# Kernel optimization log

Measured on AMD Instinct MI355X. Metric: run time of the kernel, lower is better.

Reference implementation:

```python
import jax, jax.numpy as jnp
import numpy as np

K = 3  # hardcoded in DRKNN.__init__


def setup_inputs() -> dict:
    key = jax.random.key(0)
    k1, k2, k3 = jax.random.split(key, 3)
    N, Q, A, B = 100000, 1024, 8, 16
    dataTensorX = jax.random.normal(k1, (N, A, B), dtype=jnp.float32)
    dataTensorY = jax.random.normal(k2, (N, 3), dtype=jnp.float32)
    inputTensor = jax.random.normal(k3, (Q, A, B), dtype=jnp.float32)
    return {"dataTensorX": dataTensorX, "dataTensorY": dataTensorY, "inputTensor": inputTensor}


def reference(dataTensorX, dataTensorY, inputTensor):
    # Flatten feature dims (1,2) -> single feature axis F = A*B
    N = dataTensorX.shape[0]
    Q = inputTensor.shape[0]
    X = dataTensorX.reshape(N, -1)   # [N, F]
    Qf = inputTensor.reshape(Q, -1)  # [Q, F]
    # squared L2 distance via expansion: ||q||^2 - 2 q.x + ||x||^2 -> [Q, N]
    x2 = jnp.sum(X * X, axis=-1)     # [N]
    q2 = jnp.sum(Qf * Qf, axis=-1)   # [Q]
    dists = q2[:, None] - 2.0 * (Qf @ X.T) + x2[None, :]  # [Q, N]
    # k smallest distances == k largest of negated distances
    _, idx = jax.lax.top_k(-dists, K)  # idx: [Q, K] int32
    outs = dataTensorY[idx]            # [Q, K, label_dim]
    out = jnp.mean(outs, axis=1)       # [Q, label_dim]
    return out, idx
```

## Files before the change

kernel.cpp:

```cpp
#include <hip/hip_runtime.h>

#define F       128
#define TILE    128
#define QBLK    128
#define FQI     8
#define NCHUNKS 64
#define KSTEP   32
#define TOPK    3
#define NSUB_MAX 3200
#define DINF    (__builtin_inff())
#define IMAX    0x7fffffff

typedef short short8 __attribute__((ext_vector_type(8)));
typedef float f32x4  __attribute__((ext_vector_type(4)));

__device__ __forceinline__ ushort f2bf(float f) {
    uint u = __float_as_uint(f);
    uint r = (u + 0x7fffu + ((u >> 16) & 1u)) >> 16;
    return (ushort)r;
}

__device__ __forceinline__ bool lex_less(float d1, int i1, float d2, int i2) {
    return (d1 < d2) || (d1 == d2 && i1 < i2);
}

__device__ __forceinline__ void gload16(const ushort* g, ushort* l) {
    __builtin_amdgcn_global_load_lds(
        (const __attribute__((address_space(1))) uint*)g,
        (__attribute__((address_space(3))) uint*)l, 16, 0, 0);
}


__global__ void conv_kernel(const float* __restrict__ src, ushort* __restrict__ dst,
                            float* __restrict__ nrm, int rows, int rowsPad) {
    int row  = blockIdx.x * 4 + (threadIdx.x >> 6);
    int lane = threadIdx.x & 63;
    if (row >= rowsPad) return;
    if (row < rows) {
        float2 v = *reinterpret_cast<const float2*>(&src[(size_t)row * F + lane * 2]);
        ushort2 b; b.x = f2bf(v.x); b.y = f2bf(v.y);
        *reinterpret_cast<ushort2*>(&dst[(size_t)row * F + lane * 2]) = b;
        float s = v.x * v.x + v.y * v.y;
        #pragma unroll
        for (int m = 32; m >= 1; m >>= 1) s += __shfl_xor(s, m, 64);
        if (lane == 0) nrm[row] = s;
    } else {
        *reinterpret_cast<ushort2*>(&dst[(size_t)row * F + lane * 2]) = make_ushort2(0, 0);
        if (lane == 0) nrm[row] = DINF;
    }
}

__global__ __launch_bounds__(256) void knn_p1(
    const ushort* __restrict__ Xbf, const ushort* __restrict__ Qbf,
    const float* __restrict__ x2f, float* __restrict__ part,
    int NTILES, int NSUB)
{
    __shared__ ushort sX[2][16384];

    const int t   = threadIdx.x;
    const int W   = t >> 6;
    const int l   = t & 63;
    const int l15 = l & 15;
    const int g   = l >> 4;
    const int chunk = blockIdx.x;
    const int qbase = blockIdx.y * QBLK;
    const int tile0 = (int)(((long)chunk * NTILES) >> 6);
    const int tile1 = (int)(((long)(chunk + 1) * NTILES) >> 6);
    const int ntile = tile1 - tile0;

    auto stage = [&](int tile, int b) {
        const ushort* gbase = Xbf + (size_t)(tile * TILE + W * 32) * F;
        #pragma unroll
        for (int m = 0; m < 8; m++) {
            const ushort* gp = gbase + ((m & 1) * 16 + l15) * F + (m >> 1) * 32 + g * 8;
            gload16(gp, &sX[b][W * 4096 + m * 512]);
        }
    };

    stage(tile0, 0);

    short8 qf[FQI][4];
    #pragma unroll
    for (int fqi = 0; fqi < FQI; fqi++) {
        const ushort* qr = Qbf + (size_t)(qbase + fqi * 16 + l15) * F + g * 8;
        #pragma unroll
        for (int s = 0; s < 4; s++) {
            uint4 u = *reinterpret_cast<const uint4*>(qr + s * 32);
            qf[fqi][s] = *reinterpret_cast<short8*>(&u);
        }
    }

    asm volatile("s_waitcnt vmcnt(0)" ::: "memory");
    __builtin_amdgcn_sched_barrier(0);

    for (int i = 0; i < ntile; i++) {
        const int tile = tile0 + i;
        const int cb = i & 1;

        float4 xv0 = *reinterpret_cast<const float4*>(&x2f[(size_t)tile * TILE + W * 32 + g * 4]);
        float4 xv1 = *reinterpret_cast<const float4*>(&x2f[(size_t)tile * TILE + W * 32 + 16 + g * 4]);
        if (i + 1 < ntile) stage(tile + 1, cb ^ 1);

        asm volatile("s_waitcnt vmcnt(10)" ::: "memory");
        __builtin_amdgcn_sched_barrier(0);

        f32x4 acc[2][FQI];
        #pragma unroll
        for (int fm = 0; fm < 2; fm++)
            #pragma unroll
            for (int fqi = 0; fqi < FQI; fqi++)
                acc[fm][fqi] = (f32x4){0.f, 0.f, 0.f, 0.f};

        #pragma unroll
        for (int s = 0; s < 4; s++) {
            short8 af0 = *reinterpret_cast<const short8*>(
                &sX[cb][W * 4096 + (s * 2 + 0) * 512 + g * 128 + l15 * 8]);
            short8 af1 = *reinterpret_cast<const short8*>(
                &sX[cb][W * 4096 + (s * 2 + 1) * 512 + g * 128 + l15 * 8]);
            #pragma unroll
            for (int fqi = 0; fqi < FQI; fqi++) {
                acc[0][fqi] = __builtin_amdgcn_mfma_f32_16x16x32_bf16(af0, qf[fqi][s], acc[0][fqi], 0, 0, 0);
                acc[1][fqi] = __builtin_amdgcn_mfma_f32_16x16x32_bf16(af1, qf[fqi][s], acc[1][fqi], 0, 0, 0);
            }
        }

        #pragma unroll
        for (int fqi = 0; fqi < FQI; fqi++) {
            f32x4 a0 = acc[0][fqi];
            f32x4 a1 = acc[1][fqi];
            float m = fminf(fminf(fminf(fmaf(-2.f, a0[0], xv0.x), fmaf(-2.f, a0[1], xv0.y)),
                                  fminf(fmaf(-2.f, a0[2], xv0.z), fmaf(-2.f, a0[3], xv0.w))),
                            fminf(fminf(fmaf(-2.f, a1[0], xv1.x), fmaf(-2.f, a1[1], xv1.y)),
                                  fminf(fmaf(-2.f, a1[2], xv1.z), fmaf(-2.f, a1[3], xv1.w))));
            m = fminf(m, __shfl_xor(m, 16, 64));
            m = fminf(m, __shfl_xor(m, 32, 64));
            if (g == 0)
                part[(size_t)(qbase + fqi * 16 + l15) * NSUB + (tile * 4 + W)] = m;
        }
    }
}

__global__ __launch_bounds__(256) void knn_p2(
    const float* __restrict__ part, const float* __restrict__ Xf,
    const float* __restrict__ x2f, const float* __restrict__ Qf,
    const float* __restrict__ q2f, const float* __restrict__ Y,
    float* __restrict__ out, int NSUB, int qTotal, int Nreal)
{
    __shared__ float spart[NSUB_MAX];
    __shared__ float sq[F];
    __shared__ float rd3[4][3];
    __shared__ int   scnt;
    __shared__ int   slist[256];
    __shared__ float wrd[4][3];
    __shared__ int   wri[4][3];

    const int t = threadIdx.x, w = t >> 6, l = t & 63;
    const int q = blockIdx.x;

    if (t < 64)
        *reinterpret_cast<float2*>(&sq[t * 2]) =
            *reinterpret_cast<const float2*>(&Qf[(size_t)q * F + t * 2]);
    if (t == 0) scnt = 0;

    const size_t prow = (size_t)q * NSUB;
    for (int i = t; i < NSUB; i += 256) spart[i] = part[prow + i];
    __syncthreads();

    float a0 = DINF, a1 = DINF, a2 = DINF;
    for (int i = t; i < NSUB; i += 256) {
        float v = spart[i];
        if (v < a2) { a2 = v;
            if (a2 < a1) { float x = a2; a2 = a1; a1 = x; }
            if (a1 < a0) { float x = a1; a1 = a0; a0 = x; } }
    }
    #pragma unroll
    for (int m = 1; m < 64; m <<= 1) {
        float o0 = __shfl_xor(a0, m, 64), o1 = __shfl_xor(a1, m, 64), o2 = __shfl_xor(a2, m, 64);
        #pragma unroll
        for (int c = 0; c < 3; c++) {
            float v = (c == 0) ? o0 : (c == 1) ? o1 : o2;
            if (v < a2) { a2 = v;
                if (a2 < a1) { float x = a2; a2 = a1; a1 = x; }
                if (a1 < a0) { float x = a1; a1 = a0; a0 = x; } }
        }
    }
    if (l == 0) { rd3[w][0] = a0; rd3[w][1] = a1; rd3[w][2] = a2; }
    __syncthreads();

    float tau;
    {
        float c0 = DINF, c1 = DINF, c2 = DINF;
        #pragma unroll
        for (int ww = 0; ww < 4; ww++)
            #pragma unroll
            for (int c = 0; c < 3; c++) {
                float v = rd3[ww][c];
                if (v < c2) { c2 = v;
                    if (c2 < c1) { float x = c2; c2 = c1; c1 = x; }
                    if (c1 < c0) { float x = c1; c1 = c0; c0 = x; } }
            }
        tau = c2 + 4.5f;
    }

    for (int i = t; i < NSUB; i += 256) {
        if (spart[i] <= tau) {
            int slot = atomicAdd(&scnt, 1);
            if (slot < 256) slist[slot] = i;
        }
    }
    __syncthreads();
    const int ncand = min(scnt, 256);
    const float q2v = q2f[q];

    float b0d = DINF, b1d = DINF, b2d = DINF;
    int   b0i = IMAX, b1i = IMAX, b2i = IMAX;
    auto ins = [&](float d, int ix) {
        if (lex_less(d, ix, b2d, b2i)) {
            b2d = d; b2i = ix;
            if (lex_less(b2d, b2i, b1d, b1i)) {
                float td = b2d; b2d = b1d; b1d = td; int ti = b2i; b2i = b1i; b1i = ti; }
            if (lex_less(b1d, b1i, b0d, b0i)) {
                float td = b1d; b1d = b0d; b0d = td; int ti = b1i; b1i = b0i; b0i = ti; }
        }
    };

    const int half = l >> 5, pl = l & 31;
    for (int ci = w; ci < ncand; ci += 4) {
        int p = slist[ci] * 32 + pl;
        float s = 0.f;
        if (p < Nreal) {
            const float4* xr = reinterpret_cast<const float4*>(&Xf[(size_t)p * F + half * 64]);
            const float4* qr = reinterpret_cast<const float4*>(&sq[half * 64]);
            float s0 = 0.f, s1 = 0.f, s2 = 0.f, s3 = 0.f;
            #pragma unroll
            for (int j = 0; j < 16; j++) {
                float4 xv = xr[j], qv = qr[j];
                s0 = fmaf(xv.x, qv.x, s0); s1 = fmaf(xv.y, qv.y, s1);
                s2 = fmaf(xv.z, qv.z, s2); s3 = fmaf(xv.w, qv.w, s3);
            }
            s = (s0 + s1) + (s2 + s3);
        }
        s += __shfl_xor(s, 32, 64);
        if (l < 32 && p < Nreal) {
            float d = (q2v - 2.0f * s) + x2f[p];
            ins(d, p);
        }
    }

    #pragma unroll
    for (int m = 1; m < 64; m <<= 1) {
        float od0 = __shfl_xor(b0d, m, 64); int oi0 = __shfl_xor(b0i, m, 64);
        float od1 = __shfl_xor(b1d, m, 64); int oi1 = __shfl_xor(b1i, m, 64);
        float od2 = __shfl_xor(b2d, m, 64); int oi2 = __shfl_xor(b2i, m, 64);
        ins(od0, oi0); ins(od1, oi1); ins(od2, oi2);
    }
    if (l == 0) {
        wrd[w][0] = b0d; wrd[w][1] = b1d; wrd[w][2] = b2d;
        wri[w][0] = b0i; wri[w][1] = b1i; wri[w][2] = b2i;
    }
    __syncthreads();

    if (t == 0) {
        #pragma unroll
        for (int ww = 1; ww < 4; ww++)
            #pragma unroll
            for (int c = 0; c < 3; c++)
                ins(wrd[ww][c], wri[ww][c]);
        int idx_off = qTotal * 3;
        #pragma unroll
        for (int c = 0; c < 3; c++) {
            float s = Y[(size_t)b0i * 3 + c] + Y[(size_t)b1i * 3 + c] + Y[(size_t)b2i * 3 + c];
            out[q * 3 + c] = s / 3.0f;
        }
        out[idx_off + q * 3 + 0] = (float)b0i;
        out[idx_off + q * 3 + 1] = (float)b1i;
        out[idx_off + q * 3 + 2] = (float)b2i;
    }
}


__global__ void fb_rownorm(const float* __restrict__ src, float* __restrict__ dst, int rows) {
    int row  = blockIdx.x * 4 + (threadIdx.x >> 6);
    int lane = threadIdx.x & 63;
    if (row >= rows) return;
    float2 v = *reinterpret_cast<const float2*>(&src[(size_t)row * F + lane * 2]);
    float s = v.x * v.x + v.y * v.y;
    #pragma unroll
    for (int m = 32; m >= 1; m >>= 1) s += __shfl_xor(s, m, 64);
    if (lane == 0) dst[row] = s;
}

__global__ __launch_bounds__(256) void fb_phase1(
    const float* __restrict__ X, const float* __restrict__ Qm,
    const float* __restrict__ x2, const float* __restrict__ q2,
    float* __restrict__ part_d, int* __restrict__ part_i,
    int N, int ntiles)
{
    __shared__ __align__(16) union {
        struct { float a[KSTEP * TILE]; float b[KSTEP * TILE]; } s;
        struct { float d[TILE][16][TOPK]; int i[TILE][16][TOPK]; } r;
    } u;

    const int t  = threadIdx.x;
    const int tx = t & 15;
    const int ty = t >> 4;
    const int chunk = blockIdx.x;
    const int qbase = blockIdx.y * TILE;
    const int ar0 = ty * 4;
    const int bc0 = tx * 4;
    const int srow0 = t >> 2;
    const int skc0  = t & 3;

    float t3d[8][TOPK];
    int   t3i[8][TOPK];
    #pragma unroll
    for (int i = 0; i < 8; i++)
        #pragma unroll
        for (int c = 0; c < TOPK; c++) { t3d[i][c] = DINF; t3i[i][c] = IMAX; }

    float q2r[8];
    #pragma unroll
    for (int i = 0; i < 8; i++) {
        int r = (i < 4) ? (ar0 + i) : (64 + ar0 + i - 4);
        q2r[i] = q2[qbase + r];
    }

    for (int tile = chunk; tile < ntiles; tile += NCHUNKS) {
        float acc[8][8];
        #pragma unroll
        for (int i = 0; i < 8; i++)
            #pragma unroll
            for (int j = 0; j < 8; j++) acc[i][j] = 0.0f;

        for (int ks = 0; ks < F; ks += KSTEP) {
            __syncthreads();
            #pragma unroll
            for (int lq = 0; lq < 4; lq++) {
                int row = srow0 | ((lq >> 1) << 6);
                int kc  = skc0 | ((lq & 1) << 2);
                int sw  = (kc & 3) << 3;
                int base = (kc * 4) * TILE + (row ^ sw);

                float4 va = *reinterpret_cast<const float4*>(
                    &Qm[(size_t)(qbase + row) * F + ks + kc * 4]);
                u.s.a[base + 0 * TILE] = va.x;
                u.s.a[base + 1 * TILE] = va.y;
                u.s.a[base + 2 * TILE] = va.z;
                u.s.a[base + 3 * TILE] = va.w;

                int n = tile * TILE + row;
                float4 vb = make_float4(0.f, 0.f, 0.f, 0.f);
                if (n < N) vb = *reinterpret_cast<const float4*>(
                    &X[(size_t)n * F + ks + kc * 4]);
                u.s.b[base + 0 * TILE] = vb.x;
                u.s.b[base + 1 * TILE] = vb.y;
                u.s.b[base + 2 * TILE] = vb.z;
                u.s.b[base + 3 * TILE] = vb.w;
            }
            __syncthreads();

            #pragma unroll
            for (int kk = 0; kk < KSTEP; kk++) {
                int sw = ((kk >> 2) & 3) << 3;
                float4 a0 = *reinterpret_cast<const float4*>(&u.s.a[kk * TILE + (ar0 ^ sw)]);
                float4 a1 = *reinterpret_cast<const float4*>(&u.s.a[kk * TILE + 64 + (ar0 ^ sw)]);
                float4 b0 = *reinterpret_cast<const float4*>(&u.s.b[kk * TILE + (bc0 ^ sw)]);
                float4 b1 = *reinterpret_cast<const float4*>(&u.s.b[kk * TILE + 64 + (bc0 ^ sw)]);
                float av[8] = {a0.x, a0.y, a0.z, a0.w, a1.x, a1.y, a1.z, a1.w};
                float bv[8] = {b0.x, b0.y, b0.z, b0.w, b1.x, b1.y, b1.z, b1.w};
                #pragma unroll
                for (int i = 0; i < 8; i++)
                    #pragma unroll
                    for (int j = 0; j < 8; j++)
                        acc[i][j] = fmaf(av[i], bv[j], acc[i][j]);
            }
        }

        #pragma unroll
        for (int j = 0; j < 8; j++) {
            int n = tile * TILE + ((j < 4) ? (bc0 + j) : (64 + bc0 + j - 4));
            if (n < N) {
                float xc = x2[n];
                #pragma unroll
                for (int i = 0; i < 8; i++) {
                    float d = (q2r[i] - 2.0f * acc[i][j]) + xc;
                    if (d < t3d[i][2]) {
                        t3d[i][2] = d; t3i[i][2] = n;
                        if (t3d[i][2] < t3d[i][1]) {
                            float td = t3d[i][2]; t3d[i][2] = t3d[i][1]; t3d[i][1] = td;
                            int ti = t3i[i][2]; t3i[i][2] = t3i[i][1]; t3i[i][1] = ti;
                        }
                        if (t3d[i][1] < t3d[i][0]) {
                            float td = t3d[i][1]; t3d[i][1] = t3d[i][0]; t3d[i][0] = td;
                            int ti = t3i[i][1]; t3i[i][1] = t3i[i][0]; t3i[i][0] = ti;
                        }
                    }
                }
            }
        }
    }

    __syncthreads();
    #pragma unroll
    for (int i = 0; i < 8; i++) {
        int r = (i < 4) ? (ar0 + i) : (64 + ar0 + i - 4);
        #pragma unroll
        for (int c = 0; c < TOPK; c++) {
            u.r.d[r][tx][c] = t3d[i][c];
            u.r.i[r][tx][c] = t3i[i][c];
        }
    }
    __syncthreads();

    if (t < TILE) {
        int row = t;
        float b0d = DINF, b1d = DINF, b2d = DINF;
        int   b0i = IMAX, b1i = IMAX, b2i = IMAX;
        for (int s = 0; s < 16; s++) {
            #pragma unroll
            for (int c = 0; c < TOPK; c++) {
                float d = u.r.d[row][s][c];
                int  ix = u.r.i[row][s][c];
                if (lex_less(d, ix, b2d, b2i)) {
                    b2d = d; b2i = ix;
                    if (lex_less(b2d, b2i, b1d, b1i)) {
                        float td = b2d; b2d = b1d; b1d = td;
                        int ti = b2i; b2i = b1i; b1i = ti;
                    }
                    if (lex_less(b1d, b1i, b0d, b0i)) {
                        float td = b1d; b1d = b0d; b0d = td;
                        int ti = b1i; b1i = b0i; b0i = ti;
                    }
                }
            }
        }
        size_t base = ((size_t)(qbase + row) * NCHUNKS + chunk) * TOPK;
        part_d[base + 0] = b0d; part_d[base + 1] = b1d; part_d[base + 2] = b2d;
        part_i[base + 0] = b0i; part_i[base + 1] = b1i; part_i[base + 2] = b2i;
    }
}

__global__ void fb_phase2(const float* __restrict__ part_d, const int* __restrict__ part_i,
                          const float* __restrict__ Y, float* __restrict__ out, int Q)
{
    int q    = blockIdx.x * 4 + (threadIdx.x >> 6);
    int lane = threadIdx.x & 63;
    if (q >= Q) return;

    float b0d = DINF, b1d = DINF, b2d = DINF;
    int   b0i = IMAX, b1i = IMAX, b2i = IMAX;

    auto ins = [&](float d, int ix) {
        if (lex_less(d, ix, b2d, b2i)) {
            b2d = d; b2i = ix;
            if (lex_less(b2d, b2i, b1d, b1i)) {
                float td = b2d; b2d = b1d; b1d = td;
                int ti = b2i; b2i = b1i; b1i = ti;
            }
            if (lex_less(b1d, b1i, b0d, b0i)) {
                float td = b1d; b1d = b0d; b0d = td;
                int ti = b1i; b1i = b0i; b0i = ti;
            }
        }
    };

    const int total = NCHUNKS * TOPK;
    size_t base = (size_t)q * total;
    for (int e = lane; e < total; e += 64)
        ins(part_d[base + e], part_i[base + e]);

    #pragma unroll
    for (int m = 1; m < 64; m <<= 1) {
        float od0 = __shfl_xor(b0d, m, 64); int oi0 = __shfl_xor(b0i, m, 64);
        float od1 = __shfl_xor(b1d, m, 64); int oi1 = __shfl_xor(b1i, m, 64);
        float od2 = __shfl_xor(b2d, m, 64); int oi2 = __shfl_xor(b2i, m, 64);
        ins(od0, oi0); ins(od1, oi1); ins(od2, oi2);
    }

    if (lane == 0) {
        int idx_off = Q * 3;
        #pragma unroll
        for (int c = 0; c < 3; c++) {
            float s = Y[(size_t)b0i * 3 + c] + Y[(size_t)b1i * 3 + c] + Y[(size_t)b2i * 3 + c];
            out[q * 3 + c] = s / 3.0f;
        }
        out[idx_off + q * 3 + 0] = (float)b0i;
        out[idx_off + q * 3 + 1] = (float)b1i;
        out[idx_off + q * 3 + 2] = (float)b2i;
    }
}


extern "C" void kernel_launch(void* const* d_in, const int* in_sizes, int n_in,
                              void* d_out, int out_size, void* d_ws, size_t ws_size,
                              hipStream_t stream) {
    const float* Xf = (const float*)d_in[0];
    const float* Y  = (const float*)d_in[1];
    const float* Qf = (const float*)d_in[2];
    int N = in_sizes[1] / 3;
    int Q = in_sizes[2] / F;
    int NTILES = (N + TILE - 1) / TILE;
    int NPAD   = NTILES * TILE;
    int NSUB   = NTILES * 4;
    char* ws = (char*)d_ws;
    (void)n_in; (void)out_size;

    size_t oA = 0;
    auto allocA = [&](size_t b) { size_t r = oA; oA = (oA + b + 255) & ~(size_t)255; return r; };
    size_t off_Xbf  = allocA((size_t)NPAD * F * 2);
    size_t off_Qbf  = allocA((size_t)Q * F * 2);
    size_t off_x2   = allocA((size_t)NPAD * 4);
    size_t off_q2   = allocA((size_t)Q * 4);
    size_t off_part = allocA((size_t)NSUB * Q * 4);

    bool okA = (oA <= ws_size) && (NSUB <= NSUB_MAX) && ((Q % QBLK) == 0);

    if (okA) {
        ushort* Xbf  = (ushort*)(ws + off_Xbf);
        ushort* Qbf  = (ushort*)(ws + off_Qbf);
        float*  x2f  = (float*) (ws + off_x2);
        float*  q2f  = (float*) (ws + off_q2);
        float*  part = (float*) (ws + off_part);

        hipLaunchKernelGGL(conv_kernel, dim3(NPAD / 4), dim3(256), 0, stream, Xf, Xbf, x2f, N, NPAD);
        hipLaunchKernelGGL(conv_kernel, dim3(Q / 4),    dim3(256), 0, stream, Qf, Qbf, q2f, Q, Q);
        hipLaunchKernelGGL(knn_p1, dim3(NCHUNKS, Q / QBLK), dim3(256), 0, stream,
                           Xbf, Qbf, x2f, part, NTILES, NSUB);
        hipLaunchKernelGGL(knn_p2, dim3(Q), dim3(256), 0, stream,
                           part, Xf, x2f, Qf, q2f, Y, (float*)d_out, NSUB, Q, N);
    } else {
        size_t oB = 0;
        auto allocB = [&](size_t b) { size_t r = oB; oB = (oB + b + 255) & ~(size_t)255; return r; };
        float* x2     = (float*)(ws + allocB((size_t)N * 4));
        float* q2     = (float*)(ws + allocB((size_t)Q * 4));
        float* part_d = (float*)(ws + allocB((size_t)Q * NCHUNKS * TOPK * 4));
        int*   part_i = (int*)  (ws + allocB((size_t)Q * NCHUNKS * TOPK * 4));

        hipLaunchKernelGGL(fb_rownorm, dim3((N + 3) / 4), dim3(256), 0, stream, Xf, x2, N);
        hipLaunchKernelGGL(fb_rownorm, dim3((Q + 3) / 4), dim3(256), 0, stream, Qf, q2, Q);
        hipLaunchKernelGGL(fb_phase1, dim3(NCHUNKS, Q / TILE), dim3(256), 0, stream,
                           Xf, Qf, x2, q2, part_d, part_i, N, NTILES);
        hipLaunchKernelGGL(fb_phase2, dim3((Q + 3) / 4), dim3(256), 0, stream,
                           part_d, part_i, Y, (float*)d_out, Q);
    }
}
```

Baseline: 126.7 us.

## Halve query block, buffer partial minima in LDS, drop double buffering

Halves the query block per workgroup (QBLK 128 to 64, FQI 8 to 4), which doubles the grid and cuts accumulator register use. Partial minima are now kept in a shared-memory table and written to global in one coalesced pass at the end, replacing scattered per-tile stores. The asynchronous double-buffered X staging becomes a single buffer with barriers around each load, so loads no longer overlap the MFMA compute. A host guard limits tiles per chunk so the LDS table fits.

```diff
diff --git a/kernel.cpp b/kernel.cpp
--- a/kernel.cpp
+++ b/kernel.cpp
@@ -2,12 +2,14 @@
 
 #define F       128
 #define TILE    128
-#define QBLK    128
-#define FQI     8
+#define QBLK    64
+#define FQI     4
 #define NCHUNKS 64
 #define KSTEP   32
 #define TOPK    3
 #define NSUB_MAX 3200
+#define SMW     57
+#define MAXCT   14
 #define DINF    (__builtin_inff())
 #define IMAX    0x7fffffff
 
@@ -55,7 +57,8 @@
     const float* __restrict__ x2f, float* __restrict__ part,
     int NTILES, int NSUB)
 {
-    __shared__ ushort sX[2][16384];
+    __shared__ ushort sX[16384];
+    __shared__ float  smin[QBLK][SMW];
 
     const int t   = threadIdx.x;
     const int W   = t >> 6;
@@ -68,18 +71,18 @@
     const int tile1 = (int)(((long)(chunk + 1) * NTILES) >> 6);
     const int ntile = tile1 - tile0;
 
-    auto stage = [&](int tile, int b) {
+    auto stage = [&](int tile) {
         const ushort* gbase = Xbf + (size_t)(tile * TILE + W * 32) * F;
         #pragma unroll
         for (int m = 0; m < 8; m++) {
             const ushort* gp = gbase + ((m & 1) * 16 + l15) * F + (m >> 1) * 32 + g * 8;
-            gload16(gp, &sX[b][W * 4096 + m * 512]);
+            gload16(gp, &sX[W * 4096 + m * 512]);
         }
     };
 
-    stage(tile0, 0);
-
     short8 qf[FQI][4];
+
+    stage(tile0);
     #pragma unroll
     for (int fqi = 0; fqi < FQI; fqi++) {
         const ushort* qr = Qbf + (size_t)(qbase + fqi * 16 + l15) * F + g * 8;
@@ -89,20 +92,13 @@
             qf[fqi][s] = *reinterpret_cast<short8*>(&u);
         }
     }
-
-    asm volatile("s_waitcnt vmcnt(0)" ::: "memory");
-    __builtin_amdgcn_sched_barrier(0);
+    __syncthreads();
 
     for (int i = 0; i < ntile; i++) {
         const int tile = tile0 + i;
-        const int cb = i & 1;
 
         float4 xv0 = *reinterpret_cast<const float4*>(&x2f[(size_t)tile * TILE + W * 32 + g * 4]);
         float4 xv1 = *reinterpret_cast<const float4*>(&x2f[(size_t)tile * TILE + W * 32 + 16 + g * 4]);
-        if (i + 1 < ntile) stage(tile + 1, cb ^ 1);
-
-        asm volatile("s_waitcnt vmcnt(10)" ::: "memory");
-        __builtin_amdgcn_sched_barrier(0);
 
         f32x4 acc[2][FQI];
         #pragma unroll
@@ -114,9 +110,9 @@
         #pragma unroll
         for (int s = 0; s < 4; s++) {
             short8 af0 = *reinterpret_cast<const short8*>(
-                &sX[cb][W * 4096 + (s * 2 + 0) * 512 + g * 128 + l15 * 8]);
+                &sX[W * 4096 + (s * 2 + 0) * 512 + g * 128 + l15 * 8]);
             short8 af1 = *reinterpret_cast<const short8*>(
-                &sX[cb][W * 4096 + (s * 2 + 1) * 512 + g * 128 + l15 * 8]);
+                &sX[W * 4096 + (s * 2 + 1) * 512 + g * 128 + l15 * 8]);
             #pragma unroll
             for (int fqi = 0; fqi < FQI; fqi++) {
                 acc[0][fqi] = __builtin_amdgcn_mfma_f32_16x16x32_bf16(af0, qf[fqi][s], acc[0][fqi], 0, 0, 0);
@@ -135,8 +131,20 @@
             m = fminf(m, __shfl_xor(m, 16, 64));
             m = fminf(m, __shfl_xor(m, 32, 64));
             if (g == 0)
-                part[(size_t)(qbase + fqi * 16 + l15) * NSUB + (tile * 4 + W)] = m;
-        }
+                smin[fqi * 16 + l15][i * 4 + W] = m;
+        }
+
+        __syncthreads();
+        if (i + 1 < ntile) stage(tile + 1);
+        __syncthreads();
+    }
+
+    const int cw = ntile * 4;
+    const int col0 = tile0 * 4;
+    for (int idx = t; idx < QBLK * cw; idx += 256) {
+        int r = idx / cw;
+        int c = idx - r * cw;
+        part[(size_t)(qbase + r) * NSUB + (col0 + c)] = smin[r][c];
     }
 }
 
@@ -513,7 +521,8 @@
     size_t off_q2   = allocA((size_t)Q * 4);
     size_t off_part = allocA((size_t)NSUB * Q * 4);
 
-    bool okA = (oA <= ws_size) && (NSUB <= NSUB_MAX) && ((Q % QBLK) == 0);
+    bool okA = (oA <= ws_size) && (NSUB <= NSUB_MAX) && ((Q % QBLK) == 0)
+            && ((NTILES + NCHUNKS - 1) / NCHUNKS <= MAXCT);
 
     if (okA) {
         ushort* Xbf  = (ushort*)(ws + off_Xbf);
```

Result: slower. 138.4 us (+9.2%).
